# Kernel optimization log

Hardware: AMD Instinct MI355X
Metric: run time of the kernel (lower is better)

Reference implementation:

```python
import jax, jax.numpy as jnp
import numpy as np

EMBED_DIM = 512
NUM_HEADS = 8
HEAD_DIM = EMBED_DIM // NUM_HEADS  # 64


def setup_inputs() -> dict:
    key = jax.random.key(0)
    ks = jax.random.split(key, 7)
    B, S, E = 4, 2048, EMBED_DIM
    std = 1.0 / np.sqrt(E)
    return {
        "x": jax.random.normal(ks[0], (B, S, E), dtype=jnp.float32),
        "wq": jax.random.uniform(ks[1], (E, E), jnp.float32, -std, std),
        "bq": jax.random.uniform(ks[2], (E,), jnp.float32, -std, std),
        "wk": jax.random.uniform(ks[3], (E, E), jnp.float32, -std, std),
        "bk": jax.random.uniform(ks[4], (E,), jnp.float32, -std, std),
        "wv": jax.random.uniform(ks[5], (E, E), jnp.float32, -std, std),
        "bv": jax.random.uniform(ks[6], (E,), jnp.float32, -std, std),
    }


def reference(x, wq, bq, wk, bk, wv, bv):
    B, S, E = x.shape
    H, D = NUM_HEADS, HEAD_DIM
    scaling = D ** (-0.5)

    def split_heads(t):  # [B,S,E] -> [B,H,S,D]
        return t.reshape(B, S, H, D).transpose(0, 2, 1, 3)

    q = split_heads(x @ wq + bq)
    k = split_heads(x @ wk + bk)
    v = split_heads(x @ wv + bv)

    # NOTE: original torch code DIVIDES by scaling (== multiply by sqrt(D)).
    scores = jnp.einsum("bhqd,bhkd->bhqk", q, k) / scaling
    weights = jax.nn.softmax(scores, axis=-1)
    ctx = jnp.einsum("bhqk,bhkd->bhqd", weights, v)  # [B,H,S,D]
    return ctx.transpose(0, 2, 1, 3).reshape(B, S, E)
```

## Files before the change

### kernel.cpp

```cpp
#include <hip/hip_runtime.h>
#include <hip/hip_bf16.h>


#define SE 2048
#define EB 512
#define BB 4
#define HH 8
#define DD 64
#define BHN (BB*HH)

typedef __attribute__((ext_vector_type(8))) short short8;
typedef __attribute__((ext_vector_type(4))) float f32x4;

#define MFMA16(a, b, c) __builtin_amdgcn_mfma_f32_16x16x32_bf16((a), (b), (c), 0, 0, 0)

#if __has_builtin(__builtin_amdgcn_exp2f)
#define EXP2(x) __builtin_amdgcn_exp2f(x)
#else
#define EXP2(x) exp2f(x)
#endif

__device__ __forceinline__ unsigned short f2bf(float f) {
    union { float f; unsigned u; } x; x.f = f;
    unsigned r = x.u + 0x7fffu + ((x.u >> 16) & 1u);
    return (unsigned short)(r >> 16);
}
__device__ __forceinline__ float bf2f(unsigned short b) {
    union { unsigned u; float f; } x; x.u = ((unsigned)b) << 16;
    return x.f;
}

__global__ void xsplit_kernel(const float* __restrict__ x,
                              unsigned short* __restrict__ xh,
                              unsigned short* __restrict__ xl, int n4) {
    int i = blockIdx.x * blockDim.x + threadIdx.x;
    if (i >= n4) return;
    float4 v = reinterpret_cast<const float4*>(x)[i];
    float f[4] = {v.x, v.y, v.z, v.w};
    ushort4 hv, lv;
    unsigned short hh[4], ll[4];
#pragma unroll
    for (int j = 0; j < 4; j++) {
        hh[j] = f2bf(f[j]);
        ll[j] = f2bf(f[j] - bf2f(hh[j]));
    }
    hv.x = hh[0]; hv.y = hh[1]; hv.z = hh[2]; hv.w = hh[3];
    lv.x = ll[0]; lv.y = ll[1]; lv.z = ll[2]; lv.w = ll[3];
    reinterpret_cast<ushort4*>(xh)[i] = hv;
    reinterpret_cast<ushort4*>(xl)[i] = lv;
}

__global__ void wsplit_kernel(const float* __restrict__ wq, const float* __restrict__ wk,
                              const float* __restrict__ wv,
                              unsigned short* __restrict__ wth,
                              unsigned short* __restrict__ wtl) {
    int tid = blockIdx.x * blockDim.x + threadIdx.x;
    if (tid >= 3 * 512 * 512) return;
    int n = tid & 511;
    int k = (tid >> 9) & 511;
    int m = tid >> 18;
    const float* w = (m == 0) ? wq : ((m == 1) ? wk : wv);
    float v = w[k * 512 + n];
    unsigned short hb = f2bf(v);
    int o = ((m * 512 + n) << 9) + k;
    wth[o] = hb;
    wtl[o] = f2bf(v - bf2f(hb));
}

__device__ __forceinline__ void stage4(const unsigned short* __restrict__ g,
                                       char* lbase, int wave, int srow, int scol,
                                       int kk) {
#pragma unroll
    for (int j = 0; j < 4; j++) {
        __builtin_amdgcn_global_load_lds(
            (const __attribute__((address_space(1))) void*)(g + (size_t)(srow + j * 8) * 512 + kk + scol),
            (__attribute__((address_space(3))) void*)(lbase + wave * 4096 + j * 1024),
            16, 0, 0);
    }
}

template <int THREE>
__global__ __launch_bounds__(256) void proj_kernel(
    const unsigned short* __restrict__ xh, const unsigned short* __restrict__ xl,
    const unsigned short* __restrict__ wth, const unsigned short* __restrict__ wtl,
    const float* __restrict__ bq, const float* __restrict__ bk, const float* __restrict__ bv,
    unsigned short* __restrict__ qh, unsigned short* __restrict__ ql,
    unsigned short* __restrict__ kh, unsigned short* __restrict__ kl,
    unsigned short* __restrict__ vt) {
    constexpr int NTILE = THREE ? 4 : 2;
    __shared__ unsigned short lds[NTILE * 8192];
    char* LB = (char*)lds;
    constexpr int AHB = 0;
    constexpr int ALB = THREE ? 16384 : 0;
    constexpr int BHB = THREE ? 32768 : 16384;
    constexpr int BLB = THREE ? 49152 : 0;

    const int lane = threadIdx.x & 63;
    const int wave = threadIdx.x >> 6;
    const int lr = lane & 15, lk = lane >> 4;
    const int mat = THREE ? blockIdx.z : 2;
    const int m0 = blockIdx.x * 128;
    const int n0 = blockIdx.y * 128;
    const int wr = wave >> 1, wc = wave & 1;

    const unsigned short* Ah = xh + (size_t)m0 * 512;
    const unsigned short* Al = xl + (size_t)m0 * 512;
    const unsigned short* Bh = wth + (size_t)(mat * 512 + n0) * 512;
    const unsigned short* Bl = wtl + (size_t)(mat * 512 + n0) * 512;

    const int srow = wave * 32 + (lane >> 3);
    const int scol = 8 * ((lane & 7) ^ (lane >> 3));
    const int swzr = (lr & 7) << 4;

    f32x4 acc[4][4];
#pragma unroll
    for (int mi = 0; mi < 4; mi++)
#pragma unroll
        for (int ni = 0; ni < 4; ni++)
#pragma unroll
            for (int r = 0; r < 4; r++) acc[mi][ni][r] = 0.f;

    for (int t = 0; t < 8; t++) {
        const int kk = t * 64;
        stage4(Ah, LB + AHB, wave, srow, scol, kk);
        if (THREE) stage4(Al, LB + ALB, wave, srow, scol, kk);
        stage4(Bh, LB + BHB, wave, srow, scol, kk);
        if (THREE) stage4(Bl, LB + BLB, wave, srow, scol, kk);
        __syncthreads();

#pragma unroll
        for (int ks = 0; ks < 2; ks++) {
            short8 ah[4], al[4], bh8[4], bl8[4];
            const int cb = (ks * 64 + lk * 16) ^ swzr;
#pragma unroll
            for (int i = 0; i < 4; i++) {
                const int ao = (wr * 64 + i * 16 + lr) * 128 + cb;
                const int bo = (wc * 64 + i * 16 + lr) * 128 + cb;
                ah[i] = *reinterpret_cast<const short8*>(LB + AHB + ao);
                if (THREE) al[i] = *reinterpret_cast<const short8*>(LB + ALB + ao);
                bh8[i] = *reinterpret_cast<const short8*>(LB + BHB + bo);
                if (THREE) bl8[i] = *reinterpret_cast<const short8*>(LB + BLB + bo);
            }
#pragma unroll
            for (int mi = 0; mi < 4; mi++)
#pragma unroll
                for (int ni = 0; ni < 4; ni++) {
                    acc[mi][ni] = MFMA16(ah[mi], bh8[ni], acc[mi][ni]);
                    if (THREE) {
                        acc[mi][ni] = MFMA16(ah[mi], bl8[ni], acc[mi][ni]);
                        acc[mi][ni] = MFMA16(al[mi], bh8[ni], acc[mi][ni]);
                    }
                }
        }
        __syncthreads();
    }

    const float* bias = THREE ? ((mat == 0) ? bq : bk) : bv;
#pragma unroll
    for (int ni = 0; ni < 4; ni++) {
        const int col = n0 + wc * 64 + ni * 16 + lr;
        const float bsv = bias[col];
        const int h = col >> 6, d = col & 63;
#pragma unroll
        for (int mi = 0; mi < 4; mi++) {
#pragma unroll
            for (int r = 0; r < 4; r++) {
                const int row = m0 + wr * 64 + mi * 16 + lk * 4 + r;
                const int b_ = row >> 11, s = row & 2047;
                const int bh_ = b_ * HH + h;
                const float val = acc[mi][ni][r] + bsv;
                if (THREE) {
                    const unsigned short hb = f2bf(val);
                    const int o = (bh_ * SE + s) * DD + d;
                    if (mat == 0) { qh[o] = hb; ql[o] = f2bf(val - bf2f(hb)); }
                    else          { kh[o] = hb; kl[o] = f2bf(val - bf2f(hb)); }
                } else {
                    vt[(bh_ * DD + d) * SE + s] = f2bf(val);
                }
            }
        }
    }
}

__global__ __launch_bounds__(256) void attn_kernel(
    const unsigned short* __restrict__ qh, const unsigned short* __restrict__ ql,
    const unsigned short* __restrict__ kh, const unsigned short* __restrict__ kl,
    const unsigned short* __restrict__ vt, float* __restrict__ out) {
    __shared__ char LB[65536];
    const int lane = threadIdx.x & 63, wave = threadIdx.x >> 6;
    const int lr = lane & 15, lk = lane >> 4;
    const int bh = blockIdx.x;
    const int b_ = bh >> 3, h = bh & 7;
    const int q0 = blockIdx.y * 128 + wave * 32;
    const int base = bh * SE * DD;
    const unsigned short* vbase = vt + bh * DD * SE;
    const float CL = 11.54156031f;
    const int swz = (lr & 7) << 4;

    const unsigned short* gp[6];
    int ginc[6], goff[6];
    {
        const int rIn = lane >> 3;
        const int c16 = (lane & 7) ^ rIn;
#pragma unroll
        for (int i = 0; i < 6; i++) {
            const int c = wave * 6 + i;
            const int mat = c >> 3, grp = c & 7;
            const int row = grp * 8 + rIn;
            if (mat == 0)      { gp[i] = kh + base + row * DD + c16 * 8;  ginc[i] = 64 * DD; }
            else if (mat == 1) { gp[i] = kl + base + row * DD + c16 * 8;  ginc[i] = 64 * DD; }
            else               { gp[i] = vbase + row * SE + c16 * 8;      ginc[i] = 64; }
            goff[i] = mat * 8192 + grp * 1024;
        }
    }

    short8 qhf[2][2], qlf[2][2];
#pragma unroll
    for (int qs = 0; qs < 2; qs++) {
        const int qoff = base + (q0 + qs * 16 + lr) * DD + lk * 8;
        qhf[qs][0] = *reinterpret_cast<const short8*>(qh + qoff);
        qhf[qs][1] = *reinterpret_cast<const short8*>(qh + qoff + 32);
        qlf[qs][0] = *reinterpret_cast<const short8*>(ql + qoff);
        qlf[qs][1] = *reinterpret_cast<const short8*>(ql + qoff + 32);
    }

    float m[2] = {-3.0e4f, -3.0e4f}, l[2] = {0.f, 0.f};
    f32x4 o[2][4];
#pragma unroll
    for (int qs = 0; qs < 2; qs++)
#pragma unroll
        for (int dnt = 0; dnt < 4; dnt++)
#pragma unroll
            for (int r = 0; r < 4; r++) o[qs][dnt][r] = 0.f;

    char* myp = LB + 49152 + wave * 4096;

#pragma unroll
    for (int i = 0; i < 6; i++) {
        __builtin_amdgcn_global_load_lds(
            (const __attribute__((address_space(1))) void*)gp[i],
            (__attribute__((address_space(3))) void*)(LB + goff[i]), 16, 0, 0);
        gp[i] += ginc[i];
    }
    __syncthreads();

    for (int kt = 0; kt < 32; kt++) {
        const char* KB = LB + (kt & 1) * 24576;
        if (kt < 31) {
            const int nb = ((kt + 1) & 1) * 24576;
#pragma unroll
            for (int i = 0; i < 6; i++) {
                __builtin_amdgcn_global_load_lds(
                    (const __attribute__((address_space(1))) void*)gp[i],
                    (__attribute__((address_space(3))) void*)(LB + nb + goff[i]), 16, 0, 0);
                gp[i] += ginc[i];
            }
        }

        f32x4 s[2][4];
#pragma unroll
        for (int qs = 0; qs < 2; qs++)
#pragma unroll
            for (int knt = 0; knt < 4; knt++)
#pragma unroll
                for (int r = 0; r < 4; r++) s[qs][knt][r] = 0.f;

        __builtin_amdgcn_s_setprio(1);
#pragma unroll
        for (int knt = 0; knt < 4; knt++) {
            const int rb = (knt * 16 + lr) * 128;
            short8 kh0 = *reinterpret_cast<const short8*>(KB + rb + ((lk * 16) ^ swz));
            short8 kh1 = *reinterpret_cast<const short8*>(KB + rb + ((64 + lk * 16) ^ swz));
            short8 kl0 = *reinterpret_cast<const short8*>(KB + 8192 + rb + ((lk * 16) ^ swz));
            short8 kl1 = *reinterpret_cast<const short8*>(KB + 8192 + rb + ((64 + lk * 16) ^ swz));
#pragma unroll
            for (int qs = 0; qs < 2; qs++) {
                s[qs][knt] = MFMA16(kh0, qhf[qs][0], s[qs][knt]);
                s[qs][knt] = MFMA16(kh1, qhf[qs][1], s[qs][knt]);
                s[qs][knt] = MFMA16(kl0, qhf[qs][0], s[qs][knt]);
                s[qs][knt] = MFMA16(kl1, qhf[qs][1], s[qs][knt]);
                s[qs][knt] = MFMA16(kh0, qlf[qs][0], s[qs][knt]);
                s[qs][knt] = MFMA16(kh1, qlf[qs][1], s[qs][knt]);
            }
        }
        __builtin_amdgcn_s_setprio(0);

        short8 vf[4][2];
#pragma unroll
        for (int dnt = 0; dnt < 4; dnt++) {
            const int rv = (dnt * 16 + lr) * 128;
            vf[dnt][0] = *reinterpret_cast<const short8*>(KB + 16384 + rv + ((lk * 16) ^ swz));
            vf[dnt][1] = *reinterpret_cast<const short8*>(KB + 16384 + rv + ((64 + lk * 16) ^ swz));
        }

#pragma unroll
        for (int qs = 0; qs < 2; qs++) {
            float mt = s[qs][0][0];
#pragma unroll
            for (int knt = 0; knt < 4; knt++)
#pragma unroll
                for (int r = 0; r < 4; r++) mt = fmaxf(mt, s[qs][knt][r]);
            mt = fmaxf(mt, __shfl_xor(mt, 16));
            mt = fmaxf(mt, __shfl_xor(mt, 32));

            if (!__all(mt <= m[qs] + 0.69314718f)) {
                const float mn = fmaxf(m[qs], mt);
                const float fac = EXP2((m[qs] - mn) * CL);
                l[qs] *= fac;
#pragma unroll
                for (int dnt = 0; dnt < 4; dnt++)
#pragma unroll
                    for (int r = 0; r < 4; r++) o[qs][dnt][r] *= fac;
                m[qs] = mn;
            }
            const float nm = -m[qs] * CL;
            float rs = 0.f;
#pragma unroll
            for (int knt = 0; knt < 4; knt++) {
                float p0 = EXP2(fmaf(s[qs][knt][0], CL, nm));
                float p1 = EXP2(fmaf(s[qs][knt][1], CL, nm));
                float p2 = EXP2(fmaf(s[qs][knt][2], CL, nm));
                float p3 = EXP2(fmaf(s[qs][knt][3], CL, nm));
                rs += (p0 + p1) + (p2 + p3);
                unsigned w0 = (unsigned)f2bf(p0) | ((unsigned)f2bf(p1) << 16);
                unsigned w1 = (unsigned)f2bf(p2) | ((unsigned)f2bf(p3) << 16);
                const int cb = (knt * 32 + lk * 8) ^ swz;
                *reinterpret_cast<uint2*>(myp + qs * 2048 + lr * 128 + cb) =
                    make_uint2(w0, w1);
            }
            rs += __shfl_xor(rs, 16);
            rs += __shfl_xor(rs, 32);
            l[qs] += rs;
        }

        __builtin_amdgcn_s_setprio(1);
#pragma unroll
        for (int qs = 0; qs < 2; qs++) {
            const char* mp = myp + qs * 2048;
            short8 pa0 = *reinterpret_cast<const short8*>(mp + lr * 128 + ((lk * 16) ^ swz));
            short8 pa1 = *reinterpret_cast<const short8*>(mp + lr * 128 + ((64 + lk * 16) ^ swz));
#pragma unroll
            for (int dnt = 0; dnt < 4; dnt++) {
                o[qs][dnt] = MFMA16(vf[dnt][0], pa0, o[qs][dnt]);
                o[qs][dnt] = MFMA16(vf[dnt][1], pa1, o[qs][dnt]);
            }
        }
        __builtin_amdgcn_s_setprio(0);

        __syncthreads();
    }

#pragma unroll
    for (int qs = 0; qs < 2; qs++) {
        const float rl = 1.0f / l[qs];
        float* op = out + (size_t)(b_ * SE + q0 + qs * 16 + lr) * EB + h * DD + lk * 4;
#pragma unroll
        for (int dnt = 0; dnt < 4; dnt++) {
            float4 val;
            val.x = o[qs][dnt][0] * rl;
            val.y = o[qs][dnt][1] * rl;
            val.z = o[qs][dnt][2] * rl;
            val.w = o[qs][dnt][3] * rl;
            *reinterpret_cast<float4*>(op + dnt * 16) = val;
        }
    }
}

extern "C" void kernel_launch(void* const* d_in, const int* in_sizes, int n_in,
                              void* d_out, int out_size, void* d_ws, size_t ws_size,
                              hipStream_t stream) {
    const float* x  = (const float*)d_in[0];
    const float* wq = (const float*)d_in[1];
    const float* bq = (const float*)d_in[2];
    const float* wk = (const float*)d_in[3];
    const float* bk = (const float*)d_in[4];
    const float* wv = (const float*)d_in[5];
    const float* bv = (const float*)d_in[6];
    float* out = (float*)d_out;

    unsigned short* ws = (unsigned short*)d_ws;
    const int NX = 8192 * 512;
    const int NW = 3 * 512 * 512;
    const int NQ = BHN * SE * DD;
    unsigned short* xh  = ws;
    unsigned short* xl  = xh + NX;
    unsigned short* wth = xl + NX;
    unsigned short* wtl = wth + NW;
    unsigned short* qhp = wtl + NW;
    unsigned short* qlp = qhp + NQ;
    unsigned short* khp = qlp + NQ;
    unsigned short* klp = khp + NQ;
    unsigned short* vtp = klp + NQ;

    xsplit_kernel<<<NX / 4 / 256, 256, 0, stream>>>(x, xh, xl, NX / 4);
    wsplit_kernel<<<NW / 256, 256, 0, stream>>>(wq, wk, wv, wth, wtl);
    proj_kernel<1><<<dim3(64, 4, 2), 256, 0, stream>>>(xh, xl, wth, wtl, bq, bk, bv,
                                                       qhp, qlp, khp, klp, vtp);
    proj_kernel<0><<<dim3(64, 4), 256, 0, stream>>>(xh, xl, wth, wtl, bq, bk, bv,
                                                    qhp, qlp, khp, klp, vtp);
    attn_kernel<<<dim3(32, 16), 256, 0, stream>>>(qhp, qlp, khp, klp, vtp, out);
}
```

Baseline: 161.1 us.

## Split attention KV range across blocks and combine partial softmax results

Doubles the block size to 512 threads (8 waves, 256 queries per block), which halves per-wave K/V staging loads. It also splits the key range into two halves over a new grid z dimension, writing unnormalized partial outputs plus running max and sum to workspace, and adds a combine kernel that merges them. The P-tile LDS buffer is shrunk to one per wave and reused per query subtile, and bf16 packing now uses the library conversion. The aim is more parallelism and more K/V reuse per block, at the cost of an extra kernel launch and the fp32 round trip through global memory for the partials.

```diff
diff --git a/kernel.cpp b/kernel.cpp
--- a/kernel.cpp
+++ b/kernel.cpp
@@ -28,6 +28,11 @@
 __device__ __forceinline__ float bf2f(unsigned short b) {
     union { unsigned u; float f; } x; x.u = ((unsigned)b) << 16;
     return x.f;
+}
+__device__ __forceinline__ unsigned packbf2(float a, float b) {
+    unsigned short lo = __bfloat16_as_ushort(__float2bfloat16(a));
+    unsigned short hi = __bfloat16_as_ushort(__float2bfloat16(b));
+    return (unsigned)lo | ((unsigned)hi << 16);
 }
 
 __global__ void xsplit_kernel(const float* __restrict__ x,
@@ -182,35 +187,40 @@
     }
 }
 
-__global__ __launch_bounds__(256) void attn_kernel(
+template <int SPLIT>
+__global__ __launch_bounds__(512, 4) void attn_kernel(
     const unsigned short* __restrict__ qh, const unsigned short* __restrict__ ql,
     const unsigned short* __restrict__ kh, const unsigned short* __restrict__ kl,
-    const unsigned short* __restrict__ vt, float* __restrict__ out) {
+    const unsigned short* __restrict__ vt, float* __restrict__ opart,
+    float2* __restrict__ mlbuf, float* __restrict__ out) {
     __shared__ char LB[65536];
     const int lane = threadIdx.x & 63, wave = threadIdx.x >> 6;
     const int lr = lane & 15, lk = lane >> 4;
     const int bh = blockIdx.x;
     const int b_ = bh >> 3, h = bh & 7;
-    const int q0 = blockIdx.y * 128 + wave * 32;
+    const int q0 = blockIdx.y * 256 + wave * 32;
+    const int sp = SPLIT ? blockIdx.z : 0;
     const int base = bh * SE * DD;
     const unsigned short* vbase = vt + bh * DD * SE;
     const float CL = 11.54156031f;
     const int swz = (lr & 7) << 4;
-
-    const unsigned short* gp[6];
-    int ginc[6], goff[6];
+    constexpr int NT = SPLIT ? 16 : 32;
+
+    const unsigned short* gp[3];
+    int ginc[3], goff[3];
     {
         const int rIn = lane >> 3;
         const int c16 = (lane & 7) ^ rIn;
 #pragma unroll
-        for (int i = 0; i < 6; i++) {
-            const int c = wave * 6 + i;
+        for (int i = 0; i < 3; i++) {
+            const int c = wave * 3 + i;
             const int mat = c >> 3, grp = c & 7;
             const int row = grp * 8 + rIn;
             if (mat == 0)      { gp[i] = kh + base + row * DD + c16 * 8;  ginc[i] = 64 * DD; }
             else if (mat == 1) { gp[i] = kl + base + row * DD + c16 * 8;  ginc[i] = 64 * DD; }
             else               { gp[i] = vbase + row * SE + c16 * 8;      ginc[i] = 64; }
             goff[i] = mat * 8192 + grp * 1024;
+            gp[i] += (size_t)(sp * NT) * ginc[i];
         }
     }
 
@@ -233,10 +243,10 @@
 #pragma unroll
             for (int r = 0; r < 4; r++) o[qs][dnt][r] = 0.f;
 
-    char* myp = LB + 49152 + wave * 4096;
-
-#pragma unroll
-    for (int i = 0; i < 6; i++) {
+    char* myp = LB + 49152 + wave * 2048;
+
+#pragma unroll
+    for (int i = 0; i < 3; i++) {
         __builtin_amdgcn_global_load_lds(
             (const __attribute__((address_space(1))) void*)gp[i],
             (__attribute__((address_space(3))) void*)(LB + goff[i]), 16, 0, 0);
@@ -244,12 +254,12 @@
     }
     __syncthreads();
 
-    for (int kt = 0; kt < 32; kt++) {
+    for (int kt = 0; kt < NT; kt++) {
         const char* KB = LB + (kt & 1) * 24576;
-        if (kt < 31) {
+        if (kt < NT - 1) {
             const int nb = ((kt + 1) & 1) * 24576;
 #pragma unroll
-            for (int i = 0; i < 6; i++) {
+            for (int i = 0; i < 3; i++) {
                 __builtin_amdgcn_global_load_lds(
                     (const __attribute__((address_space(1))) void*)gp[i],
                     (__attribute__((address_space(3))) void*)(LB + nb + goff[i]), 16, 0, 0);
@@ -322,47 +332,84 @@
                 float p2 = EXP2(fmaf(s[qs][knt][2], CL, nm));
                 float p3 = EXP2(fmaf(s[qs][knt][3], CL, nm));
                 rs += (p0 + p1) + (p2 + p3);
-                unsigned w0 = (unsigned)f2bf(p0) | ((unsigned)f2bf(p1) << 16);
-                unsigned w1 = (unsigned)f2bf(p2) | ((unsigned)f2bf(p3) << 16);
+                unsigned w0 = packbf2(p0, p1);
+                unsigned w1 = packbf2(p2, p3);
                 const int cb = (knt * 32 + lk * 8) ^ swz;
-                *reinterpret_cast<uint2*>(myp + qs * 2048 + lr * 128 + cb) =
-                    make_uint2(w0, w1);
+                *reinterpret_cast<uint2*>(myp + lr * 128 + cb) = make_uint2(w0, w1);
             }
             rs += __shfl_xor(rs, 16);
             rs += __shfl_xor(rs, 32);
             l[qs] += rs;
-        }
-
-        __builtin_amdgcn_s_setprio(1);
-#pragma unroll
-        for (int qs = 0; qs < 2; qs++) {
-            const char* mp = myp + qs * 2048;
-            short8 pa0 = *reinterpret_cast<const short8*>(mp + lr * 128 + ((lk * 16) ^ swz));
-            short8 pa1 = *reinterpret_cast<const short8*>(mp + lr * 128 + ((64 + lk * 16) ^ swz));
+
+            short8 pa0 = *reinterpret_cast<const short8*>(myp + lr * 128 + ((lk * 16) ^ swz));
+            short8 pa1 = *reinterpret_cast<const short8*>(myp + lr * 128 + ((64 + lk * 16) ^ swz));
+            __builtin_amdgcn_s_setprio(1);
 #pragma unroll
             for (int dnt = 0; dnt < 4; dnt++) {
                 o[qs][dnt] = MFMA16(vf[dnt][0], pa0, o[qs][dnt]);
                 o[qs][dnt] = MFMA16(vf[dnt][1], pa1, o[qs][dnt]);
             }
-        }
-        __builtin_amdgcn_s_setprio(0);
+            __builtin_amdgcn_s_setprio(0);
+        }
 
         __syncthreads();
     }
 
-#pragma unroll
-    for (int qs = 0; qs < 2; qs++) {
-        const float rl = 1.0f / l[qs];
-        float* op = out + (size_t)(b_ * SE + q0 + qs * 16 + lr) * EB + h * DD + lk * 4;
-#pragma unroll
-        for (int dnt = 0; dnt < 4; dnt++) {
-            float4 val;
-            val.x = o[qs][dnt][0] * rl;
-            val.y = o[qs][dnt][1] * rl;
-            val.z = o[qs][dnt][2] * rl;
-            val.w = o[qs][dnt][3] * rl;
-            *reinterpret_cast<float4*>(op + dnt * 16) = val;
-        }
+    if (SPLIT) {
+        float* ob = opart + (size_t)(bh * 2 + sp) * 2048 * 64;
+        float2* mlb = mlbuf + (size_t)(bh * 2 + sp) * 2048;
+#pragma unroll
+        for (int qs = 0; qs < 2; qs++) {
+            const int q = q0 + qs * 16 + lr;
+            float* op = ob + (size_t)q * 64 + lk * 4;
+#pragma unroll
+            for (int dnt = 0; dnt < 4; dnt++) {
+                float4 val;
+                val.x = o[qs][dnt][0]; val.y = o[qs][dnt][1];
+                val.z = o[qs][dnt][2]; val.w = o[qs][dnt][3];
+                *reinterpret_cast<float4*>(op + dnt * 16) = val;
+            }
+            if (lk == 0) mlb[q] = make_float2(m[qs], l[qs]);
+        }
+    } else {
+#pragma unroll
+        for (int qs = 0; qs < 2; qs++) {
+            const float rl = 1.0f / l[qs];
+            float* op = out + (size_t)(b_ * SE + q0 + qs * 16 + lr) * EB + h * DD + lk * 4;
+#pragma unroll
+            for (int dnt = 0; dnt < 4; dnt++) {
+                float4 val;
+                val.x = o[qs][dnt][0] * rl;
+                val.y = o[qs][dnt][1] * rl;
+                val.z = o[qs][dnt][2] * rl;
+                val.w = o[qs][dnt][3] * rl;
+                *reinterpret_cast<float4*>(op + dnt * 16) = val;
+            }
+        }
+    }
+}
+
+__global__ __launch_bounds__(64) void combine_kernel(
+    const float* __restrict__ opart, const float2* __restrict__ mlbuf,
+    float* __restrict__ out) {
+    const int g = blockIdx.x;
+    const int bh = g >> 6, qc = g & 63;
+    const int b_ = bh >> 3, h = bh & 7;
+    const int lane = threadIdx.x;
+    const float CL = 11.54156031f;
+    const float* o0 = opart + (size_t)(bh * 2) * 2048 * 64 + (size_t)qc * 32 * 64;
+    const float* o1 = o0 + (size_t)2048 * 64;
+    const float2* ml0 = mlbuf + (size_t)(bh * 2) * 2048 + qc * 32;
+    const float2* ml1 = ml0 + 2048;
+#pragma unroll 4
+    for (int i = 0; i < 32; i++) {
+        const float2 a = ml0[i], b = ml1[i];
+        const float M = fmaxf(a.x, b.x);
+        const float e0 = EXP2((a.x - M) * CL);
+        const float e1 = EXP2((b.x - M) * CL);
+        const float rd = 1.0f / (e0 * a.y + e1 * b.y);
+        const float val = (e0 * o0[i * 64 + lane] + e1 * o1[i * 64 + lane]) * rd;
+        out[(size_t)(b_ * SE + qc * 32 + i) * EB + h * DD + lane] = val;
     }
 }
 
@@ -391,6 +438,12 @@
     unsigned short* khp = qlp + NQ;
     unsigned short* klp = khp + NQ;
     unsigned short* vtp = klp + NQ;
+    const size_t bf16_elems = (size_t)2 * NX + 2 * NW + 5 * NQ;
+    float* opart = (float*)(ws + bf16_elems);
+    float2* mlbuf = (float2*)(opart + (size_t)32 * 2 * 2048 * 64);
+    const size_t need_bytes = bf16_elems * 2
+                            + (size_t)32 * 2 * 2048 * 64 * 4
+                            + (size_t)32 * 2 * 2048 * 8;
 
     xsplit_kernel<<<NX / 4 / 256, 256, 0, stream>>>(x, xh, xl, NX / 4);
     wsplit_kernel<<<NW / 256, 256, 0, stream>>>(wq, wk, wv, wth, wtl);
@@ -398,5 +451,12 @@
                                                        qhp, qlp, khp, klp, vtp);
     proj_kernel<0><<<dim3(64, 4), 256, 0, stream>>>(xh, xl, wth, wtl, bq, bk, bv,
                                                     qhp, qlp, khp, klp, vtp);
-    attn_kernel<<<dim3(32, 16), 256, 0, stream>>>(qhp, qlp, khp, klp, vtp, out);
-}
+    if (ws_size >= need_bytes) {
+        attn_kernel<1><<<dim3(32, 8, 2), 512, 0, stream>>>(qhp, qlp, khp, klp, vtp,
+                                                           opart, mlbuf, out);
+        combine_kernel<<<2048, 64, 0, stream>>>(opart, mlbuf, out);
+    } else {
+        attn_kernel<0><<<dim3(32, 8), 512, 0, stream>>>(qhp, qlp, khp, klp, vtp,
+                                                        nullptr, nullptr, out);
+    }
+}
```

Result: slower. 235.8 us (+46.4%).

## Split attention key tiles across wave pairs with flash-decoding style merge

Applied to the files above, without the earlier changes.

Doubles the attention block to 512 threads so that each pair of waves shares one 32-query group and each wave covers half of every 64-key tile. Each wave keeps its own softmax state, and the two partial outputs are merged through LDS at the end using max/sum rescaling. This gives more waves per CU and fewer registers per wave, which should help hide latency. The cost is extra syncs, an LDS exchange epilogue, and each wave computing softmax statistics over fewer keys per tile. It also swaps the manual bf16 rounding for the library conversion intrinsic.

```diff
diff --git a/kernel.cpp b/kernel.cpp
--- a/kernel.cpp
+++ b/kernel.cpp
@@ -28,6 +28,11 @@
 __device__ __forceinline__ float bf2f(unsigned short b) {
     union { unsigned u; float f; } x; x.u = ((unsigned)b) << 16;
     return x.f;
+}
+__device__ __forceinline__ unsigned packbf2(float a, float b) {
+    unsigned short lo = __bfloat16_as_ushort(__float2bfloat16(a));
+    unsigned short hi = __bfloat16_as_ushort(__float2bfloat16(b));
+    return (unsigned)lo | ((unsigned)hi << 16);
 }
 
 __global__ void xsplit_kernel(const float* __restrict__ x,
@@ -182,29 +187,30 @@
     }
 }
 
-__global__ __launch_bounds__(256) void attn_kernel(
+__global__ __launch_bounds__(512, 4) void attn_kernel(
     const unsigned short* __restrict__ qh, const unsigned short* __restrict__ ql,
     const unsigned short* __restrict__ kh, const unsigned short* __restrict__ kl,
     const unsigned short* __restrict__ vt, float* __restrict__ out) {
     __shared__ char LB[65536];
     const int lane = threadIdx.x & 63, wave = threadIdx.x >> 6;
     const int lr = lane & 15, lk = lane >> 4;
+    const int qg = wave >> 1, khf = wave & 1;
     const int bh = blockIdx.x;
     const int b_ = bh >> 3, h = bh & 7;
-    const int q0 = blockIdx.y * 128 + wave * 32;
+    const int q0 = blockIdx.y * 128 + qg * 32;
     const int base = bh * SE * DD;
     const unsigned short* vbase = vt + bh * DD * SE;
     const float CL = 11.54156031f;
     const int swz = (lr & 7) << 4;
 
-    const unsigned short* gp[6];
-    int ginc[6], goff[6];
+    const unsigned short* gp[3];
+    int ginc[3], goff[3];
     {
         const int rIn = lane >> 3;
         const int c16 = (lane & 7) ^ rIn;
 #pragma unroll
-        for (int i = 0; i < 6; i++) {
-            const int c = wave * 6 + i;
+        for (int i = 0; i < 3; i++) {
+            const int c = wave * 3 + i;
             const int mat = c >> 3, grp = c & 7;
             const int row = grp * 8 + rIn;
             if (mat == 0)      { gp[i] = kh + base + row * DD + c16 * 8;  ginc[i] = 64 * DD; }
@@ -233,10 +239,10 @@
 #pragma unroll
             for (int r = 0; r < 4; r++) o[qs][dnt][r] = 0.f;
 
-    char* myp = LB + 49152 + wave * 4096;
-
-#pragma unroll
-    for (int i = 0; i < 6; i++) {
+    char* myp = LB + 49152 + wave * 2048;
+
+#pragma unroll
+    for (int i = 0; i < 3; i++) {
         __builtin_amdgcn_global_load_lds(
             (const __attribute__((address_space(1))) void*)gp[i],
             (__attribute__((address_space(3))) void*)(LB + goff[i]), 16, 0, 0);
@@ -249,7 +255,7 @@
         if (kt < 31) {
             const int nb = ((kt + 1) & 1) * 24576;
 #pragma unroll
-            for (int i = 0; i < 6; i++) {
+            for (int i = 0; i < 3; i++) {
                 __builtin_amdgcn_global_load_lds(
                     (const __attribute__((address_space(1))) void*)gp[i],
                     (__attribute__((address_space(3))) void*)(LB + nb + goff[i]), 16, 0, 0);
@@ -257,18 +263,18 @@
             }
         }
 
-        f32x4 s[2][4];
+        f32x4 s[2][2];
 #pragma unroll
         for (int qs = 0; qs < 2; qs++)
 #pragma unroll
-            for (int knt = 0; knt < 4; knt++)
+            for (int knt = 0; knt < 2; knt++)
 #pragma unroll
                 for (int r = 0; r < 4; r++) s[qs][knt][r] = 0.f;
 
         __builtin_amdgcn_s_setprio(1);
 #pragma unroll
-        for (int knt = 0; knt < 4; knt++) {
-            const int rb = (knt * 16 + lr) * 128;
+        for (int knt = 0; knt < 2; knt++) {
+            const int rb = (khf * 32 + knt * 16 + lr) * 128;
             short8 kh0 = *reinterpret_cast<const short8*>(KB + rb + ((lk * 16) ^ swz));
             short8 kh1 = *reinterpret_cast<const short8*>(KB + rb + ((64 + lk * 16) ^ swz));
             short8 kl0 = *reinterpret_cast<const short8*>(KB + 8192 + rb + ((lk * 16) ^ swz));
@@ -285,21 +291,18 @@
         }
         __builtin_amdgcn_s_setprio(0);
 
-        short8 vf[4][2];
+        short8 vf[4];
 #pragma unroll
         for (int dnt = 0; dnt < 4; dnt++) {
             const int rv = (dnt * 16 + lr) * 128;
-            vf[dnt][0] = *reinterpret_cast<const short8*>(KB + 16384 + rv + ((lk * 16) ^ swz));
-            vf[dnt][1] = *reinterpret_cast<const short8*>(KB + 16384 + rv + ((64 + lk * 16) ^ swz));
+            vf[dnt] = *reinterpret_cast<const short8*>(KB + 16384 + rv + ((khf * 64 + lk * 16) ^ swz));
         }
 
 #pragma unroll
         for (int qs = 0; qs < 2; qs++) {
-            float mt = s[qs][0][0];
-#pragma unroll
-            for (int knt = 0; knt < 4; knt++)
-#pragma unroll
-                for (int r = 0; r < 4; r++) mt = fmaxf(mt, s[qs][knt][r]);
+            float mt = fmaxf(fmaxf(s[qs][0][0], s[qs][0][1]), fmaxf(s[qs][0][2], s[qs][0][3]));
+#pragma unroll
+            for (int r = 0; r < 4; r++) mt = fmaxf(mt, s[qs][1][r]);
             mt = fmaxf(mt, __shfl_xor(mt, 16));
             mt = fmaxf(mt, __shfl_xor(mt, 32));
 
@@ -316,52 +319,69 @@
             const float nm = -m[qs] * CL;
             float rs = 0.f;
 #pragma unroll
-            for (int knt = 0; knt < 4; knt++) {
+            for (int knt = 0; knt < 2; knt++) {
                 float p0 = EXP2(fmaf(s[qs][knt][0], CL, nm));
                 float p1 = EXP2(fmaf(s[qs][knt][1], CL, nm));
                 float p2 = EXP2(fmaf(s[qs][knt][2], CL, nm));
                 float p3 = EXP2(fmaf(s[qs][knt][3], CL, nm));
                 rs += (p0 + p1) + (p2 + p3);
-                unsigned w0 = (unsigned)f2bf(p0) | ((unsigned)f2bf(p1) << 16);
-                unsigned w1 = (unsigned)f2bf(p2) | ((unsigned)f2bf(p3) << 16);
+                unsigned w0 = packbf2(p0, p1);
+                unsigned w1 = packbf2(p2, p3);
                 const int cb = (knt * 32 + lk * 8) ^ swz;
-                *reinterpret_cast<uint2*>(myp + qs * 2048 + lr * 128 + cb) =
-                    make_uint2(w0, w1);
+                *reinterpret_cast<uint2*>(myp + lr * 128 + cb) = make_uint2(w0, w1);
             }
             rs += __shfl_xor(rs, 16);
             rs += __shfl_xor(rs, 32);
             l[qs] += rs;
-        }
-
-        __builtin_amdgcn_s_setprio(1);
+
+            short8 pa = *reinterpret_cast<const short8*>(myp + lr * 128 + ((lk * 16) ^ swz));
+            __builtin_amdgcn_s_setprio(1);
+#pragma unroll
+            for (int dnt = 0; dnt < 4; dnt++)
+                o[qs][dnt] = MFMA16(vf[dnt], pa, o[qs][dnt]);
+            __builtin_amdgcn_s_setprio(0);
+        }
+
+        __syncthreads();
+    }
+
+    float* exo = (float*)(LB) + qg * 2048;
+    float2* exm = (float2*)(LB + 32768) + qg * 32;
+    if (khf == 1) {
 #pragma unroll
         for (int qs = 0; qs < 2; qs++) {
-            const char* mp = myp + qs * 2048;
-            short8 pa0 = *reinterpret_cast<const short8*>(mp + lr * 128 + ((lk * 16) ^ swz));
-            short8 pa1 = *reinterpret_cast<const short8*>(mp + lr * 128 + ((64 + lk * 16) ^ swz));
+            float* op = exo + (qs * 16 + lr) * 64 + lk * 4;
 #pragma unroll
             for (int dnt = 0; dnt < 4; dnt++) {
-                o[qs][dnt] = MFMA16(vf[dnt][0], pa0, o[qs][dnt]);
-                o[qs][dnt] = MFMA16(vf[dnt][1], pa1, o[qs][dnt]);
-            }
-        }
-        __builtin_amdgcn_s_setprio(0);
-
-        __syncthreads();
-    }
-
-#pragma unroll
-    for (int qs = 0; qs < 2; qs++) {
-        const float rl = 1.0f / l[qs];
-        float* op = out + (size_t)(b_ * SE + q0 + qs * 16 + lr) * EB + h * DD + lk * 4;
-#pragma unroll
-        for (int dnt = 0; dnt < 4; dnt++) {
-            float4 val;
-            val.x = o[qs][dnt][0] * rl;
-            val.y = o[qs][dnt][1] * rl;
-            val.z = o[qs][dnt][2] * rl;
-            val.w = o[qs][dnt][3] * rl;
-            *reinterpret_cast<float4*>(op + dnt * 16) = val;
+                float4 val;
+                val.x = o[qs][dnt][0]; val.y = o[qs][dnt][1];
+                val.z = o[qs][dnt][2]; val.w = o[qs][dnt][3];
+                *reinterpret_cast<float4*>(op + dnt * 16) = val;
+            }
+            if (lk == 0) exm[qs * 16 + lr] = make_float2(m[qs], l[qs]);
+        }
+    }
+    __syncthreads();
+    if (khf == 0) {
+#pragma unroll
+        for (int qs = 0; qs < 2; qs++) {
+            const float2 ml1 = exm[qs * 16 + lr];
+            const float M = fmaxf(m[qs], ml1.x);
+            const float f0 = EXP2((m[qs] - M) * CL);
+            const float f1 = EXP2((ml1.x - M) * CL);
+            const float rl = 1.0f / (f0 * l[qs] + f1 * ml1.y);
+            const float* ip = exo + (qs * 16 + lr) * 64 + lk * 4;
+            float* op = out + (size_t)(b_ * SE + q0 + qs * 16 + lr) * EB + h * DD + lk * 4;
+#pragma unroll
+            for (int dnt = 0; dnt < 4; dnt++) {
+                float4 o1 = *reinterpret_cast<const float4*>(ip + dnt * 16);
+                float4 val;
+                val.x = (f0 * o[qs][dnt][0] + f1 * o1.x) * rl;
+                val.y = (f0 * o[qs][dnt][1] + f1 * o1.y) * rl;
+                val.z = (f0 * o[qs][dnt][2] + f1 * o1.z) * rl;
+                val.w = (f0 * o[qs][dnt][3] + f1 * o1.w) * rl;
+                *reinterpret_cast<float4*>(op + dnt * 16) = val;
+            }
         }
     }
 }
@@ -398,5 +418,5 @@
                                                        qhp, qlp, khp, klp, vtp);
     proj_kernel<0><<<dim3(64, 4), 256, 0, stream>>>(xh, xl, wth, wtl, bq, bk, bv,
                                                     qhp, qlp, khp, klp, vtp);
-    attn_kernel<<<dim3(32, 16), 256, 0, stream>>>(qhp, qlp, khp, klp, vtp, out);
-}
+    attn_kernel<<<dim3(32, 16), 512, 0, stream>>>(qhp, qlp, khp, klp, vtp, out);
+}
```

After: 153.5 us (median of 2 runs). -4.7%, faster.
